# Performance work log

Hardware: AMD Instinct MI355X
Metric: run time of the kernel (lower is better)

Reference implementation:

```python
import jax, jax.numpy as jnp
import numpy as np

# RCGANConfig constants
D_X, D_EPS = 64, 16
A_VOCAB, A_EMB = 100, 32
T_VOCAB, T_EMB = 4, 16
D_H = 128
D_IN = A_EMB + T_EMB + D_X + D_EPS + 1  # 129 (use_prev_y adds 1)


def setup_inputs() -> dict:
    key = jax.random.key(0)
    ks = jax.random.split(key, 20)
    B, T = 1024, 256
    s = 0.05
    x = jax.random.normal(ks[0], (B, D_X), jnp.float32)
    a = jax.random.randint(ks[1], (B, T), 0, A_VOCAB, jnp.int32)
    t = jax.random.randint(ks[2], (B, T), 0, T_VOCAB, jnp.int32)
    y = (jax.random.uniform(ks[3], (B, T)) < 0.5).astype(jnp.float32)
    mask = jnp.ones((B, T), jnp.float32)
    eps = jax.random.normal(ks[4], (B, T, D_EPS), jnp.float32)
    # parameters
    Wx = jax.random.normal(ks[5], (D_X, D_X), jnp.float32) * s
    bx = jnp.zeros((D_X,), jnp.float32)
    Ea = jax.random.normal(ks[6], (A_VOCAB, A_EMB), jnp.float32) * s
    Et = jax.random.normal(ks[7], (T_VOCAB, T_EMB), jnp.float32) * s
    Wih = jax.random.normal(ks[8], (3 * D_H, D_IN), jnp.float32) * s
    Whh = jax.random.normal(ks[9], (3 * D_H, D_H), jnp.float32) * s
    bih = jnp.zeros((3 * D_H,), jnp.float32)
    bhh = jnp.zeros((3 * D_H,), jnp.float32)
    W0 = jax.random.normal(ks[10], (D_H, D_X + D_EPS), jnp.float32) * s
    b0 = jnp.zeros((D_H,), jnp.float32)
    Wy = jax.random.normal(ks[11], (1, D_H), jnp.float32) * s
    by = jnp.zeros((1,), jnp.float32)
    return {"x": x, "a": a, "t": t, "y": y, "mask": mask, "eps": eps,
            "Wx": Wx, "bx": bx, "Ea": Ea, "Et": Et, "Wih": Wih, "Whh": Whh,
            "bih": bih, "bhh": bhh, "W0": W0, "b0": b0, "Wy": Wy, "by": by}


def reference(x, a, t, y, mask, eps, Wx, bx, Ea, Et, Wih, Whh, bih, bhh, W0, b0, Wy, by):
    # teacher_forcing path, rnn='gru', use_prev_y=True, y provided, stochastic_y=False
    B, T = a.shape
    x_enc = x @ Wx.T + bx                                        # [B, d_x] (constant per step)
    h0 = jnp.tanh(jnp.concatenate([x_enc, eps[:, 0, :]], -1) @ W0.T + b0)  # [B, d_h]
    # prev_y: zeros at t=0, then detached teacher signal y[:, t-1]
    prev_y = jnp.concatenate(
        [jnp.zeros((B, 1), y.dtype), jax.lax.stop_gradient(y[:, :-1])], axis=1)[..., None]  # [B,T,1]
    a_enc = Ea[a]                                                # [B,T,a_emb]
    t_enc = Et[t]                                                # [B,T,t_emb]
    inp = jnp.concatenate(
        [a_enc, t_enc, jnp.broadcast_to(x_enc[:, None, :], (B, T, x_enc.shape[-1])), eps, prev_y],
        axis=-1)                                                 # [B,T,d_in]
    gates_x = inp @ Wih.T + bih                                  # [B,T,3*d_h] precomputed input gates

    def step(h, gx):
        gh = h @ Whh.T + bhh
        gx_r, gx_z, gx_n = jnp.split(gx, 3, axis=-1)
        gh_r, gh_z, gh_n = jnp.split(gh, 3, axis=-1)
        r = jax.nn.sigmoid(gx_r + gh_r)
        z = jax.nn.sigmoid(gx_z + gh_z)
        n = jnp.tanh(gx_n + r * gh_n)
        h_new = (1.0 - z) * n + z * h
        return h_new, h_new

    _, hs = jax.lax.scan(step, h0, jnp.swapaxes(gates_x, 0, 1))  # hs: [T,B,d_h]
    hs = jnp.swapaxes(hs, 0, 1)                                  # [B,T,d_h]
    logits = hs @ Wy.T + by                                      # [B,T,1]
    prob = jax.nn.sigmoid(logits)
    m = mask[..., None]
    logits_o = m * logits + (1.0 - m) * jax.lax.stop_gradient(logits)
    y_o = m * prob + (1.0 - m) * jax.lax.stop_gradient(prob)
    # stacked: [..., 0] = y_logits, [..., 1] = y
    return jnp.concatenate([logits_o, y_o], axis=-1)             # [B,T,2]
```

## Files before the change

### kernel.cpp

```cpp
#include <hip/hip_runtime.h>
#include <hip/hip_bf16.h>

typedef __attribute__((ext_vector_type(8))) short bfrag;
typedef __attribute__((ext_vector_type(4))) float ffrag;

#define NB 1024
#define NT 256

static __device__ __forceinline__ float fast_rcp(float x) { return __builtin_amdgcn_rcpf(x); }
static __device__ __forceinline__ float sigm(float x) {
  return fast_rcp(1.f + __builtin_amdgcn_exp2f(-1.44269504f * x));
}
static __device__ __forceinline__ float tanh_f(float x) {
  return __builtin_fmaf(2.f, fast_rcp(1.f + __builtin_amdgcn_exp2f(-2.88539008f * x)), -1.f);
}
static __device__ __forceinline__ float bf2f(__hip_bfloat16 v) { return __bfloat162float(v); }
static __device__ __forceinline__ short f2bs(float f) {
  __hip_bfloat16 h = __float2bfloat16(f);
  return *reinterpret_cast<short*>(&h);
}
static __device__ __forceinline__ void barrier_lgkm() {
  asm volatile("s_waitcnt lgkmcnt(0)\n\ts_barrier" ::: "memory");
}

__global__ __launch_bounds__(512, 2) void gru_kernel(
    const float* __restrict__ x,
    const int* __restrict__ a_ids,
    const int* __restrict__ t_ids,
    const float* __restrict__ y,
    const float* __restrict__ eps,
    const float* __restrict__ Wx,
    const float* __restrict__ bx,
    const float* __restrict__ Ea,
    const float* __restrict__ Et,
    const float* __restrict__ Wih,
    const float* __restrict__ Whh,
    const float* __restrict__ bih,
    const float* __restrict__ bhh,
    const float* __restrict__ W0,
    const float* __restrict__ b0g,
    const float* __restrict__ Wy,
    const float* __restrict__ by,
    float* __restrict__ out)
{
  __shared__ __align__(16) __hip_bfloat16 h_bf[2][16][136];
  __shared__ __align__(16) __hip_bfloat16 ind_s[2][16][72];
  __shared__ __align__(16) __hip_bfloat16 Ea_s[100][32];
  __shared__ __align__(16) __hip_bfloat16 Et_s[4][16];
  __shared__ float prevy_s[2][16];
  __shared__ float bsum_r[128], bsum_z[128], bihn_s[128], bhhn_s[128];
  __shared__ float wprev_s[384];
  __shared__ __align__(16) char uni[38912];
  unsigned short* aid_s   = (unsigned short*)(uni);
  unsigned short* tix_s   = (unsigned short*)(uni + 8192);
  __hip_bfloat16* eps_ch  = (__hip_bfloat16*)(uni + 16384);
  float*          y_ch    = (float*)(uni + 32768);
  float*          out_b   = (float*)(uni + 34816);
  __hip_bfloat16* Wxb     = (__hip_bfloat16*)(uni);
  __hip_bfloat16* W0b     = (__hip_bfloat16*)(uni + 8192);
  float*          x_s     = (float*)(uni + 28672);
  float*          eps0s   = (float*)(uni + 32832);
  float*          xe_s    = (float*)(uni + 33920);
  float*          h0f     = (float*)(uni);

  const int tid = threadIdx.x;
  const int w = tid >> 6, l = tid & 63;
  const int lmod = l & 15, ldiv = l >> 4;
  const int i_own = 16 * w + lmod;
  const int b0 = blockIdx.x * 16;

  if (tid < 128) {
    bsum_r[tid] = bih[tid] + bhh[tid];
    bsum_z[tid] = bih[128 + tid] + bhh[128 + tid];
    bihn_s[tid] = bih[256 + tid];
    bhhn_s[tid] = bhh[256 + tid];
  }
  if (tid < 384) wprev_s[tid] = Wih[tid * 129 + 128];
  for (int j = tid; j < 3200; j += 512) ((__hip_bfloat16*)Ea_s)[j] = __float2bfloat16(Ea[j]);
  if (tid < 64) ((__hip_bfloat16*)Et_s)[tid] = __float2bfloat16(Et[tid]);
  for (int j = tid; j < 4096; j += 512)  Wxb[j] = __float2bfloat16(Wx[j]);
  for (int j = tid; j < 10240; j += 512) W0b[j] = __float2bfloat16(W0[j]);
  for (int j = tid; j < 1024; j += 512) {
    int r = j >> 6, c = j & 63;
    x_s[r * 65 + c] = x[(b0 + r) * 64 + c];
  }
  if (tid < 256) {
    int r = tid >> 4, c = tid & 15;
    eps0s[r * 17 + c] = eps[((b0 + r) * NT) * 16 + c];
  }
  const float by_f = by[0];

  bfrag Bh[3][4], Bi[3][2];
  #pragma unroll
  for (int g = 0; g < 3; g++) {
    int n = (g * 8 + w) * 16 + lmod;
    #pragma unroll
    for (int kc = 0; kc < 4; kc++) {
      int k = kc * 32 + ldiv * 8;
      const float* wh = Whh + n * 128 + k;
      float4 h0v = *reinterpret_cast<const float4*>(wh);
      float4 h1v = *reinterpret_cast<const float4*>(wh + 4);
      bfrag th = {f2bs(h0v.x), f2bs(h0v.y), f2bs(h0v.z), f2bs(h0v.w),
                  f2bs(h1v.x), f2bs(h1v.y), f2bs(h1v.z), f2bs(h1v.w)};
      Bh[g][kc] = th;
    }
    #pragma unroll
    for (int kc = 0; kc < 2; kc++) {
      bfrag ti;
      #pragma unroll
      for (int j = 0; j < 8; j++) {
        int dk = kc * 32 + ldiv * 8 + j;
        int col = dk < 48 ? dk : dk + 64;
        ti[j] = f2bs(Wih[n * 129 + col]);
      }
      Bi[g][kc] = ti;
    }
  }
  bfrag Bl[4];
  if (w == 7) {
    #pragma unroll
    for (int kc = 0; kc < 4; kc++) {
      bfrag bt;
      #pragma unroll
      for (int j = 0; j < 8; j++)
        bt[j] = (lmod == 0) ? f2bs(Wy[kc * 32 + ldiv * 8 + j]) : (short)0;
      Bl[kc] = bt;
    }
  }
  __syncthreads();

  for (int j = tid; j < 1024; j += 512) {
    int r = j & 15, i = j >> 4;
    float acc = bx[i];
    #pragma unroll 8
    for (int k = 0; k < 64; k++) acc += x_s[r * 65 + k] * bf2f(Wxb[i * 64 + k]);
    xe_s[r * 65 + i] = acc;
    h_bf[1][r][i] = __float2bfloat16(acc);
  }
  __syncthreads();

  for (int j = tid; j < 2048; j += 512) {
    int r = j & 15, o = j >> 4;
    float acc = b0g[o];
    #pragma unroll 8
    for (int k = 0; k < 64; k++) acc += xe_s[r * 65 + k] * bf2f(W0b[o * 80 + k]);
    #pragma unroll
    for (int k = 0; k < 16; k++) acc += eps0s[r * 17 + k] * bf2f(W0b[o * 80 + 64 + k]);
    h0f[r * 128 + o] = tanh_f(acc);
  }

  ffrag gxc[3];
  {
    ffrag z = {0.f, 0.f, 0.f, 0.f};
    gxc[0] = z; gxc[1] = z; gxc[2] = z;
    #pragma unroll
    for (int kc = 0; kc < 2; kc++) {
      bfrag axd = *reinterpret_cast<const bfrag*>(&h_bf[1][lmod][kc * 32 + ldiv * 8]);
      #pragma unroll
      for (int g = 0; g < 3; g++) {
        int n = (g * 8 + w) * 16 + lmod;
        const float* wi = Wih + n * 129 + 48 + kc * 32 + ldiv * 8;
        bfrag bt;
        #pragma unroll
        for (int j = 0; j < 8; j++) bt[j] = f2bs(wi[j]);
        gxc[g] = __builtin_amdgcn_mfma_f32_16x16x32_bf16(axd, bt, gxc[g], 0, 0, 0);
      }
    }
    float brf = bsum_r[i_own], bzf = bsum_z[i_own], bn1 = bihn_s[i_own];
    #pragma unroll
    for (int q = 0; q < 4; q++) {
      gxc[0][q] += brf;
      gxc[1][q] += bzf;
      gxc[2][q] += bn1;
    }
  }
  __syncthreads();

  float h_reg[4];
  #pragma unroll
  for (int q = 0; q < 4; q++) {
    int row = ldiv * 4 + q;
    float hv = h0f[row * 128 + i_own];
    h_reg[q] = hv;
    h_bf[0][row][i_own] = __float2bfloat16(hv);
  }
  __syncthreads();

  for (int j = tid; j < 4096; j += 512) {
    int r = j >> 8, t = j & 255;
    aid_s[r * 256 + t] = (unsigned short)a_ids[(b0 + r) * NT + t];
    tix_s[r * 256 + t] = (unsigned short)t_ids[(b0 + r) * NT + t];
  }
  {
    int r = tid >> 5, sub = tid & 31;
    const float* p = eps + ((b0 + r) * NT + 0) * 16 + sub * 8;
    float4 eA = *reinterpret_cast<const float4*>(p);
    float4 eB = *reinterpret_cast<const float4*>(p + 4);
    int toff = sub >> 1, c8 = (sub & 1) * 8;
    bfrag e = {f2bs(eA.x), f2bs(eA.y), f2bs(eA.z), f2bs(eA.w),
               f2bs(eB.x), f2bs(eB.y), f2bs(eB.z), f2bs(eB.w)};
    *reinterpret_cast<bfrag*>(&eps_ch[(toff * 16 + r) * 16 + c8]) = e;
    if (tid < 64) {
      int r2 = tid >> 2, s2 = tid & 3;
      float4 yv = *reinterpret_cast<const float4*>(y + (b0 + r2) * NT + s2 * 4);
      *reinterpret_cast<float4*>(&y_ch[r2 * 16 + s2 * 4]) = yv;
    }
  }
  if (tid < 16) prevy_s[0][tid] = 0.f;
  __syncthreads();

  if (tid >= 256 && tid < 384) {
    int j = tid - 256, r = j >> 3, c = j & 7;
    bfrag e;
    if (c < 4)      e = *reinterpret_cast<const bfrag*>(&Ea_s[aid_s[r * 256]][c * 8]);
    else if (c < 6) e = *reinterpret_cast<const bfrag*>(&Et_s[tix_s[r * 256]][(c - 4) * 8]);
    else            e = *reinterpret_cast<const bfrag*>(&eps_ch[(r) * 16 + (c - 6) * 8]);
    *reinterpret_cast<bfrag*>(&ind_s[0][r][c * 8]) = e;
  }
  const float wpr = wprev_s[i_own], wpz = wprev_s[128 + i_own], wpn = wprev_s[256 + i_own];
  const float bn2 = bhhn_s[i_own];
  __syncthreads();

  for (int t = 0; t < NT; t++) {
    const int buf = t & 1, nbuf = buf ^ 1;

    if ((t & 15) == 1 && t > 16 && tid < 128) {
      int fc = (t - 17) >> 4;
      int r = tid >> 3, k = tid & 7;
      int s = fc * 16 + 2 * k, slot = s & 31;
      float4 v;
      v.x = out_b[slot * 32 + r * 2];
      v.y = out_b[slot * 32 + r * 2 + 1];
      v.z = out_b[(slot + 1) * 32 + r * 2];
      v.w = out_b[(slot + 1) * 32 + r * 2 + 1];
      *reinterpret_cast<float4*>(out + ((b0 + r) * NT + s) * 2) = v;
    }

    const bool ck = ((t & 15) == 0) && (t + 16 < NT);
    float4 eA, eB, yv;
    const int cr = tid >> 5, csub = tid & 31;
    if (ck) {
      const float* p = eps + ((b0 + cr) * NT + t + 16) * 16 + csub * 8;
      eA = *reinterpret_cast<const float4*>(p);
      eB = *reinterpret_cast<const float4*>(p + 4);
      if (tid < 64) {
        int r2 = tid >> 2, s2 = tid & 3;
        yv = *reinterpret_cast<const float4*>(y + (b0 + r2) * NT + t + 16 + s2 * 4);
      }
    }

    const int t1 = (t + 1 < NT) ? t + 1 : NT - 1;
    if (tid >= 256 && tid < 384) {
      int j = tid - 256, r = j >> 3, c = j & 7;
      bfrag e;
      if (c < 4)      e = *reinterpret_cast<const bfrag*>(&Ea_s[aid_s[r * 256 + t1]][c * 8]);
      else if (c < 6) e = *reinterpret_cast<const bfrag*>(&Et_s[tix_s[r * 256 + t1]][(c - 4) * 8]);
      else            e = *reinterpret_cast<const bfrag*>(
                          &eps_ch[((((t1 >> 4) & 1) * 16 + (t1 & 15)) * 16 + r) * 16 + (c - 6) * 8]);
      *reinterpret_cast<bfrag*>(&ind_s[nbuf][r][c * 8]) = e;
    }
    if (tid >= 384 && tid < 400) {
      int r = tid - 384;
      prevy_s[nbuf][r] = y_ch[((t >> 4) & 1) * 256 + r * 16 + (t & 15)];
    }

    ffrag ar = gxc[0], az = gxc[1], anx = gxc[2], anh, agl;
    #pragma unroll
    for (int q = 0; q < 4; q++) anh[q] = bn2;
    #pragma unroll
    for (int kc = 0; kc < 2; kc++) {
      bfrag ax = *reinterpret_cast<const bfrag*>(&ind_s[buf][lmod][kc * 32 + ldiv * 8]);
      ar  = __builtin_amdgcn_mfma_f32_16x16x32_bf16(ax, Bi[0][kc], ar, 0, 0, 0);
      az  = __builtin_amdgcn_mfma_f32_16x16x32_bf16(ax, Bi[1][kc], az, 0, 0, 0);
      anx = __builtin_amdgcn_mfma_f32_16x16x32_bf16(ax, Bi[2][kc], anx, 0, 0, 0);
    }
    if (w == 7) {
      #pragma unroll
      for (int q = 0; q < 4; q++) agl[q] = by_f;
    }
    #pragma unroll
    for (int kc = 0; kc < 4; kc++) {
      bfrag ah = *reinterpret_cast<const bfrag*>(&h_bf[buf][lmod][kc * 32 + ldiv * 8]);
      ar  = __builtin_amdgcn_mfma_f32_16x16x32_bf16(ah, Bh[0][kc], ar, 0, 0, 0);
      az  = __builtin_amdgcn_mfma_f32_16x16x32_bf16(ah, Bh[1][kc], az, 0, 0, 0);
      anh = __builtin_amdgcn_mfma_f32_16x16x32_bf16(ah, Bh[2][kc], anh, 0, 0, 0);
      if (w == 7)
        agl = __builtin_amdgcn_mfma_f32_16x16x32_bf16(ah, Bl[kc], agl, 0, 0, 0);
    }

    if (w == 7 && t > 0 && lmod == 0) {
      int slot = (t - 1) & 31;
      #pragma unroll
      for (int q = 0; q < 4; q++) {
        int row = ldiv * 4 + q;
        float lg = agl[q];
        out_b[slot * 32 + row * 2]     = lg;
        out_b[slot * 32 + row * 2 + 1] = sigm(lg);
      }
    }

    #pragma unroll
    for (int q = 0; q < 4; q++) {
      int row = ldiv * 4 + q;
      float py = prevy_s[buf][row];
      float rv = sigm(__builtin_fmaf(py, wpr, ar[q]));
      float zv = sigm(__builtin_fmaf(py, wpz, az[q]));
      float nv = tanh_f(__builtin_fmaf(py, wpn, anx[q]) + rv * anh[q]);
      float hn = __builtin_fmaf(zv, h_reg[q] - nv, nv);
      h_reg[q] = hn;
      h_bf[nbuf][row][i_own] = __float2bfloat16(hn);
    }

    if (ck) {
      int cb = ((t >> 4) + 1) & 1;
      int toff = csub >> 1, c8 = (csub & 1) * 8;
      bfrag e = {f2bs(eA.x), f2bs(eA.y), f2bs(eA.z), f2bs(eA.w),
                 f2bs(eB.x), f2bs(eB.y), f2bs(eB.z), f2bs(eB.w)};
      *reinterpret_cast<bfrag*>(&eps_ch[((cb * 16 + toff) * 16 + cr) * 16 + c8]) = e;
      if (tid < 64) {
        int r2 = tid >> 2, s2 = tid & 3;
        *reinterpret_cast<float4*>(&y_ch[cb * 256 + r2 * 16 + s2 * 4]) = yv;
      }
    }

    barrier_lgkm();
  }

  if (w == 7) {
    ffrag agl;
    #pragma unroll
    for (int q = 0; q < 4; q++) agl[q] = by_f;
    #pragma unroll
    for (int kc = 0; kc < 4; kc++) {
      bfrag ah = *reinterpret_cast<const bfrag*>(&h_bf[0][lmod][kc * 32 + ldiv * 8]);
      agl = __builtin_amdgcn_mfma_f32_16x16x32_bf16(ah, Bl[kc], agl, 0, 0, 0);
    }
    if (lmod == 0) {
      #pragma unroll
      for (int q = 0; q < 4; q++) {
        int row = ldiv * 4 + q;
        float lg = agl[q];
        out_b[31 * 32 + row * 2]     = lg;
        out_b[31 * 32 + row * 2 + 1] = sigm(lg);
      }
    }
  }
  __syncthreads();
  if (tid < 128) {
    int r = tid >> 3, k = tid & 7;
    int s = 240 + 2 * k, slot = s & 31;
    float4 v;
    v.x = out_b[slot * 32 + r * 2];
    v.y = out_b[slot * 32 + r * 2 + 1];
    v.z = out_b[(slot + 1) * 32 + r * 2];
    v.w = out_b[(slot + 1) * 32 + r * 2 + 1];
    *reinterpret_cast<float4*>(out + ((b0 + r) * NT + s) * 2) = v;
  }
}

extern "C" void kernel_launch(void* const* d_in, const int* in_sizes, int n_in,
                              void* d_out, int out_size, void* d_ws, size_t ws_size,
                              hipStream_t stream) {
  const float* x   = (const float*)d_in[0];
  const int*   a   = (const int*)d_in[1];
  const int*   tt  = (const int*)d_in[2];
  const float* y   = (const float*)d_in[3];
  const float* eps = (const float*)d_in[5];
  const float* Wx  = (const float*)d_in[6];
  const float* bx  = (const float*)d_in[7];
  const float* Ea  = (const float*)d_in[8];
  const float* Et  = (const float*)d_in[9];
  const float* Wih = (const float*)d_in[10];
  const float* Whh = (const float*)d_in[11];
  const float* bih = (const float*)d_in[12];
  const float* bhh = (const float*)d_in[13];
  const float* W0  = (const float*)d_in[14];
  const float* b0  = (const float*)d_in[15];
  const float* Wy  = (const float*)d_in[16];
  const float* by  = (const float*)d_in[17];
  float* out = (float*)d_out;

  gru_kernel<<<NB / 16, 512, 0, stream>>>(x, a, tt, y, eps, Wx, bx, Ea, Et,
                                          Wih, Whh, bih, bhh, W0, b0, Wy, by, out);
}
```

Baseline: 368.5 us.

## Defer eps chunk store, read prev_y directly, stagger MFMA k-order per wave

Moves the LDS store of prefetched eps/y chunks to the step after the global load, so the load latency overlaps a whole step instead of stalling at the end of the step. It removes the prevy_s staging buffer: each thread reads the previous y from a bf16 y chunk in LDS, which drops one per-step LDS write. It also rotates the k-chunk order per wave to spread LDS bank accesses, and unrolls the time loop by two. The register-carried prefetch values and the bf16 y storage add register pressure but keep y exact, since y is 0 or 1.

```diff
diff --git a/kernel.cpp b/kernel.cpp
--- a/kernel.cpp
+++ b/kernel.cpp
@@ -2,6 +2,7 @@
 #include <hip/hip_bf16.h>
 
 typedef __attribute__((ext_vector_type(8))) short bfrag;
+typedef __attribute__((ext_vector_type(4))) short bhalf4;
 typedef __attribute__((ext_vector_type(4))) float ffrag;
 
 #define NB 1024
@@ -47,14 +48,13 @@
   __shared__ __align__(16) __hip_bfloat16 ind_s[2][16][72];
   __shared__ __align__(16) __hip_bfloat16 Ea_s[100][32];
   __shared__ __align__(16) __hip_bfloat16 Et_s[4][16];
-  __shared__ float prevy_s[2][16];
   __shared__ float bsum_r[128], bsum_z[128], bihn_s[128], bhhn_s[128];
   __shared__ float wprev_s[384];
   __shared__ __align__(16) char uni[38912];
   unsigned short* aid_s   = (unsigned short*)(uni);
   unsigned short* tix_s   = (unsigned short*)(uni + 8192);
   __hip_bfloat16* eps_ch  = (__hip_bfloat16*)(uni + 16384);
-  float*          y_ch    = (float*)(uni + 32768);
+  __hip_bfloat16* y_chb   = (__hip_bfloat16*)(uni + 32768);
   float*          out_b   = (float*)(uni + 34816);
   __hip_bfloat16* Wxb     = (__hip_bfloat16*)(uni);
   __hip_bfloat16* W0b     = (__hip_bfloat16*)(uni + 8192);
@@ -194,22 +194,24 @@
   {
     int r = tid >> 5, sub = tid & 31;
     const float* p = eps + ((b0 + r) * NT + 0) * 16 + sub * 8;
-    float4 eA = *reinterpret_cast<const float4*>(p);
-    float4 eB = *reinterpret_cast<const float4*>(p + 4);
+    float4 eA0 = *reinterpret_cast<const float4*>(p);
+    float4 eB0 = *reinterpret_cast<const float4*>(p + 4);
     int toff = sub >> 1, c8 = (sub & 1) * 8;
-    bfrag e = {f2bs(eA.x), f2bs(eA.y), f2bs(eA.z), f2bs(eA.w),
-               f2bs(eB.x), f2bs(eB.y), f2bs(eB.z), f2bs(eB.w)};
+    bfrag e = {f2bs(eA0.x), f2bs(eA0.y), f2bs(eA0.z), f2bs(eA0.w),
+               f2bs(eB0.x), f2bs(eB0.y), f2bs(eB0.z), f2bs(eB0.w)};
     *reinterpret_cast<bfrag*>(&eps_ch[(toff * 16 + r) * 16 + c8]) = e;
     if (tid < 64) {
       int r2 = tid >> 2, s2 = tid & 3;
-      float4 yv = *reinterpret_cast<const float4*>(y + (b0 + r2) * NT + s2 * 4);
-      *reinterpret_cast<float4*>(&y_ch[r2 * 16 + s2 * 4]) = yv;
-    }
-  }
-  if (tid < 16) prevy_s[0][tid] = 0.f;
-  __syncthreads();
-
-  if (tid >= 256 && tid < 384) {
+      float4 yv0 = *reinterpret_cast<const float4*>(y + (b0 + r2) * NT + s2 * 4);
+      bhalf4 yb = {f2bs(yv0.x), f2bs(yv0.y), f2bs(yv0.z), f2bs(yv0.w)};
+      *reinterpret_cast<bhalf4*>(&y_chb[r2 * 16 + s2 * 4]) = yb;
+    }
+  }
+  __syncthreads();
+
+  const bool do_emb = (tid >= 256 && tid < 384);
+  const int er8 = (tid - 256) >> 3, ch = (tid - 256) & 7;
+  if (do_emb) {
     int j = tid - 256, r = j >> 3, c = j & 7;
     bfrag e;
     if (c < 4)      e = *reinterpret_cast<const bfrag*>(&Ea_s[aid_s[r * 256]][c * 8]);
@@ -221,8 +223,25 @@
   const float bn2 = bhhn_s[i_own];
   __syncthreads();
 
+  float4 eA, eB, yv;
+  const int cr = tid >> 5, csub = tid & 31;
+
+  #pragma unroll 2
   for (int t = 0; t < NT; t++) {
     const int buf = t & 1, nbuf = buf ^ 1;
+
+    if ((t & 15) == 1 && t < 226) {
+      int cb = ((t >> 4) + 1) & 1;
+      int toff = csub >> 1, c8 = (csub & 1) * 8;
+      bfrag e = {f2bs(eA.x), f2bs(eA.y), f2bs(eA.z), f2bs(eA.w),
+                 f2bs(eB.x), f2bs(eB.y), f2bs(eB.z), f2bs(eB.w)};
+      *reinterpret_cast<bfrag*>(&eps_ch[((cb * 16 + toff) * 16 + cr) * 16 + c8]) = e;
+      if (tid < 64) {
+        int r2 = tid >> 2, s2 = tid & 3;
+        bhalf4 yb = {f2bs(yv.x), f2bs(yv.y), f2bs(yv.z), f2bs(yv.w)};
+        *reinterpret_cast<bhalf4*>(&y_chb[cb * 256 + r2 * 16 + s2 * 4]) = yb;
+      }
+    }
 
     if ((t & 15) == 1 && t > 16 && tid < 128) {
       int fc = (t - 17) >> 4;
@@ -236,10 +255,7 @@
       *reinterpret_cast<float4*>(out + ((b0 + r) * NT + s) * 2) = v;
     }
 
-    const bool ck = ((t & 15) == 0) && (t + 16 < NT);
-    float4 eA, eB, yv;
-    const int cr = tid >> 5, csub = tid & 31;
-    if (ck) {
+    if (((t & 15) == 0) && (t + 16 < NT)) {
       const float* p = eps + ((b0 + cr) * NT + t + 16) * 16 + csub * 8;
       eA = *reinterpret_cast<const float4*>(p);
       eB = *reinterpret_cast<const float4*>(p + 4);
@@ -250,25 +266,21 @@
     }
 
     const int t1 = (t + 1 < NT) ? t + 1 : NT - 1;
-    if (tid >= 256 && tid < 384) {
-      int j = tid - 256, r = j >> 3, c = j & 7;
+    if (do_emb) {
       bfrag e;
-      if (c < 4)      e = *reinterpret_cast<const bfrag*>(&Ea_s[aid_s[r * 256 + t1]][c * 8]);
-      else if (c < 6) e = *reinterpret_cast<const bfrag*>(&Et_s[tix_s[r * 256 + t1]][(c - 4) * 8]);
-      else            e = *reinterpret_cast<const bfrag*>(
-                          &eps_ch[((((t1 >> 4) & 1) * 16 + (t1 & 15)) * 16 + r) * 16 + (c - 6) * 8]);
-      *reinterpret_cast<bfrag*>(&ind_s[nbuf][r][c * 8]) = e;
-    }
-    if (tid >= 384 && tid < 400) {
-      int r = tid - 384;
-      prevy_s[nbuf][r] = y_ch[((t >> 4) & 1) * 256 + r * 16 + (t & 15)];
+      if (ch < 4)      e = *reinterpret_cast<const bfrag*>(&Ea_s[aid_s[er8 * 256 + t1]][ch * 8]);
+      else if (ch < 6) e = *reinterpret_cast<const bfrag*>(&Et_s[tix_s[er8 * 256 + t1]][(ch - 4) * 8]);
+      else             e = *reinterpret_cast<const bfrag*>(
+                           &eps_ch[((((t1 >> 4) & 1) * 16 + (t1 & 15)) * 16 + er8) * 16 + (ch - 6) * 8]);
+      *reinterpret_cast<bfrag*>(&ind_s[nbuf][er8][ch * 8]) = e;
     }
 
     ffrag ar = gxc[0], az = gxc[1], anx = gxc[2], anh, agl;
     #pragma unroll
     for (int q = 0; q < 4; q++) anh[q] = bn2;
     #pragma unroll
-    for (int kc = 0; kc < 2; kc++) {
+    for (int i = 0; i < 2; i++) {
+      int kc = (i + w) & 1;
       bfrag ax = *reinterpret_cast<const bfrag*>(&ind_s[buf][lmod][kc * 32 + ldiv * 8]);
       ar  = __builtin_amdgcn_mfma_f32_16x16x32_bf16(ax, Bi[0][kc], ar, 0, 0, 0);
       az  = __builtin_amdgcn_mfma_f32_16x16x32_bf16(ax, Bi[1][kc], az, 0, 0, 0);
@@ -279,7 +291,8 @@
       for (int q = 0; q < 4; q++) agl[q] = by_f;
     }
     #pragma unroll
-    for (int kc = 0; kc < 4; kc++) {
+    for (int i = 0; i < 4; i++) {
+      int kc = (i + w) & 3;
       bfrag ah = *reinterpret_cast<const bfrag*>(&h_bf[buf][lmod][kc * 32 + ldiv * 8]);
       ar  = __builtin_amdgcn_mfma_f32_16x16x32_bf16(ah, Bh[0][kc], ar, 0, 0, 0);
       az  = __builtin_amdgcn_mfma_f32_16x16x32_bf16(ah, Bh[1][kc], az, 0, 0, 0);
@@ -302,25 +315,14 @@
     #pragma unroll
     for (int q = 0; q < 4; q++) {
       int row = ldiv * 4 + q;
-      float py = prevy_s[buf][row];
+      float py = (t == 0) ? 0.f
+               : bf2f(y_chb[(((t - 1) >> 4) & 1) * 256 + row * 16 + ((t - 1) & 15)]);
       float rv = sigm(__builtin_fmaf(py, wpr, ar[q]));
       float zv = sigm(__builtin_fmaf(py, wpz, az[q]));
       float nv = tanh_f(__builtin_fmaf(py, wpn, anx[q]) + rv * anh[q]);
       float hn = __builtin_fmaf(zv, h_reg[q] - nv, nv);
       h_reg[q] = hn;
       h_bf[nbuf][row][i_own] = __float2bfloat16(hn);
-    }
-
-    if (ck) {
-      int cb = ((t >> 4) + 1) & 1;
-      int toff = csub >> 1, c8 = (csub & 1) * 8;
-      bfrag e = {f2bs(eA.x), f2bs(eA.y), f2bs(eA.z), f2bs(eA.w),
-                 f2bs(eB.x), f2bs(eB.y), f2bs(eB.z), f2bs(eB.w)};
-      *reinterpret_cast<bfrag*>(&eps_ch[((cb * 16 + toff) * 16 + cr) * 16 + c8]) = e;
-      if (tid < 64) {
-        int r2 = tid >> 2, s2 = tid & 3;
-        *reinterpret_cast<float4*>(&y_ch[cb * 256 + r2 * 16 + s2 * 4]) = yv;
-      }
     }
 
     barrier_lgkm();
```

After: 405.4 us. 1.1x slower.
